# Kernel tuning notes

Measured on AMD Instinct MI355X. Metric: run time of the kernel, lower is better.

Reference implementation:

```python
import jax, jax.numpy as jnp
import numpy as np

SEM_DIM = 256
CODEBOOK_SIZE = 8192
FSQ_LEVELS = 21  # acoustic_codebook_size
EPS = 1e-5


def setup_inputs() -> dict:
    key = jax.random.key(0)
    k1, k2, k3 = jax.random.split(key, 3)
    x = jax.random.normal(k1, (8, 292, 4096), dtype=jnp.float32)
    embedding_sum = jax.random.normal(k2, (CODEBOOK_SIZE, SEM_DIM), dtype=jnp.float32)
    cluster_usage = jax.random.uniform(k3, (CODEBOOK_SIZE,), dtype=jnp.float32)
    return {"x": x, "embedding_sum": embedding_sum, "cluster_usage": cluster_usage}


def reference(x, embedding_sum, cluster_usage):
    B, D, T = x.shape
    # Codebook embedding = EMA sum / clamped usage  (SemanticCodebook.embedding)
    emb = embedding_sum / jnp.clip(cluster_usage, EPS, None)[:, None]  # [K, S]

    # ---- semantic encode: cdist(p=2) + argmin ----
    sem = x[:, :SEM_DIM, :]                                   # [B, S, T]
    flat = jnp.transpose(sem, (0, 2, 1)).reshape(B * T, SEM_DIM)  # [BT, S]
    x2 = jnp.sum(flat * flat, axis=-1, keepdims=True)         # [BT, 1]
    e2 = jnp.sum(emb * emb, axis=-1)                          # [K]
    d2 = x2 - 2.0 * (flat @ emb.T) + e2[None, :]              # [BT, K] squared dists
    sem_codes = jnp.argmin(d2, axis=-1).reshape(B, 1, T).astype(jnp.int64)

    # ---- acoustic encode: FSQ (tanh -> scale -> round) ----
    ac = jnp.tanh(x[:, SEM_DIM:, :])                          # [B, A, T]
    scaled = (ac + 1.0) * 0.5 * (FSQ_LEVELS - 1)
    ac_codes = jnp.round(scaled).astype(jnp.int64)            # [B, A, T]

    codes = jnp.concatenate([sem_codes, ac_codes], axis=1)    # [B, 1+A, T]

    # ---- decode (round trip) ----
    sem_emb = jnp.transpose(emb[sem_codes[:, 0, :]], (0, 2, 1))      # [B, S, T]
    ac_emb = ac_codes.astype(jnp.float32) * (2.0 / (FSQ_LEVELS - 1)) - 1.0  # [B, A, T]
    recon = jnp.concatenate([sem_emb, ac_emb], axis=1)        # [B, D, T]
    return codes, recon
```

## Files before the change

kernel.cpp:

```cpp
#include <hip/hip_runtime.h>
#include <hip/hip_bf16.h>

#define SEM_DIM   256
#define CODEBOOK  8192
#define B_        8
#define T_        4096
#define D_        292
#define NCH       37
#define EPSV      1e-5f
#define NSP       4
#define KAPPA     2.05e-3f
#define D0        0.01f
#define CAP       128
#define QMAX      1536

typedef unsigned short u16;
typedef float v4f __attribute__((ext_vector_type(4)));
typedef _Float16 v8h __attribute__((ext_vector_type(8)));

constexpr int ROWS = B_ * T_;
constexpr size_t OFF_XT   = 0;
constexpr size_t OFF_ET   = 4194304;
constexpr size_t OFF_E2G  = 5242880;
constexpr size_t OFF_X2   = 5259264;
constexpr size_t OFF_CNT  = 5292032;
constexpr size_t OFF_CAND = 5324800;
constexpr size_t RECON_OFF = 1212416;

__device__ __forceinline__ u16 h16bits(float v) {
    _Float16 h = (_Float16)v;
    return *(u16*)&h;
}

__global__ __launch_bounds__(256) void init_kernel(int* __restrict__ cnt,
                                                   float* __restrict__ x2)
{
    int r = blockIdx.x * 256 + threadIdx.x;
    cnt[r] = 0;
    x2[r] = 0.f;
}

__global__ __launch_bounds__(256) void prep_emb_kernel(
    const float* __restrict__ es, const float* __restrict__ cu,
    u16* __restrict__ Et, float* __restrict__ e2f, float* __restrict__ gf)
{
    int c = blockIdx.x;
    int d = threadIdx.x;
    float denom = fmaxf(cu[c], EPSV);
    float v = es[(size_t)c * SEM_DIM + d] / denom;
    float vc = fminf(fmaxf(v, -60000.f), 60000.f);

    __shared__ u16 hbuf[256];
    hbuf[d] = h16bits(vc);

    float s = v * v;
    #pragma unroll
    for (int m = 32; m >= 1; m >>= 1) s += __shfl_xor(s, m);
    __shared__ float red[4];
    int lane = d & 63, w = d >> 6;
    if (lane == 0) red[w] = s;
    __syncthreads();

    if (d < 32) {
        uint4 pk = *(const uint4*)&hbuf[d * 8];
        size_t byt = (size_t)(c >> 6) * 32768 + (size_t)d * 1024 + (size_t)(c & 63) * 16;
        *(uint4*)((char*)Et + byt) = pk;
    }
    if (d == 0) {
        float e2 = red[0] + red[1] + red[2] + red[3];
        e2f[c] = e2;
        gf[c]  = KAPPA * sqrtf(e2);
    }
}

__global__ __launch_bounds__(256) void prep_x_kernel(
    const float* __restrict__ x, u16* __restrict__ Xt, float* __restrict__ x2)
{
    __shared__ float tile[64][65];
    int bidx = blockIdx.x;
    int dc = bidx & 3;
    int tc = (bidx >> 2) & 63;
    int b  = bidx >> 8;
    int d0 = dc * 64, t0 = tc * 64;
    int tx = threadIdx.x & 63;
    int dq = threadIdx.x >> 6;

    float part = 0.f;
    #pragma unroll
    for (int i = 0; i < 16; i++) {
        int d = dq * 16 + i;
        float v = x[((size_t)b * D_ + d0 + d) * T_ + t0 + tx];
        tile[d][tx] = v;
        part = fmaf(v, v, part);
    }
    atomicAdd(&x2[b * T_ + t0 + tx], part);
    __syncthreads();

    #pragma unroll
    for (int j = 0; j < 2; j++) {
        int lin = threadIdx.x * 2 + j;
        int tr  = lin >> 3;
        int ch  = lin & 7;
        unsigned w[4];
        #pragma unroll
        for (int p = 0; p < 4; p++) {
            float v0 = tile[ch * 8 + p * 2 + 0][tr];
            float v1 = tile[ch * 8 + p * 2 + 1][tr];
            w[p] = (unsigned)h16bits(v0) | ((unsigned)h16bits(v1) << 16);
        }
        int row = b * T_ + t0 + tr;
        int R = row >> 4, l15 = row & 15;
        int k8 = d0 / 8 + ch;
        int ks = k8 >> 2, l4 = k8 & 3;
        size_t byt = (size_t)((R * 8 + ks) * 4 + l4) * 256 + (size_t)l15 * 16;
        *(uint4*)((char*)Xt + byt) = make_uint4(w[0], w[1], w[2], w[3]);
    }
}

#define GBM 256
#define NTT (CODEBOOK / NSP / 32)

__global__ __launch_bounds__(512, 4) void gemm_emit_kernel(
    const u16* __restrict__ Xt, const u16* __restrict__ Et,
    const float* __restrict__ e2f, const float* __restrict__ gf,
    const float* __restrict__ x2,
    int* __restrict__ cnt, u16* __restrict__ cand)
{
    __shared__ u16 Bs[2][8192];
    __shared__ float e2s[2048], gs[2048];
    __shared__ unsigned qbuf[QMAX];
    __shared__ int qn;
    int tid  = threadIdx.x;
    int lane = tid & 63, wid = tid >> 6;
    int l15 = lane & 15, l4 = lane >> 4;
    int mblk = blockIdx.x >> 2, split = blockIdx.x & 3;
    int m0 = mblk * GBM;
    int cbase = split * (CODEBOOK / NSP);
    if (tid == 0) qn = 0;

    {
        int c4 = tid * 4;
        *(float4*)&e2s[c4] = *(const float4*)&e2f[cbase + c4];
        *(float4*)&gs[c4]  = *(const float4*)&gf[cbase + c4];
    }

    v8h aX[2][8];
    #pragma unroll
    for (int mfm = 0; mfm < 2; mfm++) {
        int Rb = (m0 + wid * 32 + mfm * 16) >> 4;
        #pragma unroll
        for (int ks = 0; ks < 8; ks++) {
            size_t byt = (size_t)((Rb * 8 + ks) * 4 + l4) * 256 + (size_t)l15 * 16;
            aX[mfm][ks] = *(const v8h*)((const char*)Xt + byt);
        }
    }

    float sxv[2], rvL[2];
    #pragma unroll
    for (int mfm = 0; mfm < 2; mfm++) {
        sxv[mfm] = sqrtf(x2[m0 + wid * 32 + mfm * 16 + l15]);
        rvL[mfm] = 3.4e38f;
    }

    v4f acc[2][2];
    #pragma unroll
    for (int a = 0; a < 2; a++)
        #pragma unroll
        for (int b = 0; b < 2; b++)
            acc[a][b] = (v4f){0.f, 0.f, 0.f, 0.f};

    auto stage = [&](int nt, int buf) {
        const char* src = (const char*)Et
            + (size_t)(split * 32 + (nt >> 1)) * 32768 + (size_t)(nt & 1) * 512;
        #pragma unroll
        for (int j = 0; j < 2; j++) {
            int dofs = wid * 2048 + j * 1024 + lane * 16;
            int q = dofs >> 9;
            int o = (dofs >> 4) & 31;
            __builtin_amdgcn_global_load_lds(
                (const __attribute__((address_space(1))) unsigned*)(src + q * 1024 + o * 16),
                (__attribute__((address_space(3))) unsigned*)((char*)&Bs[buf][0] + dofs),
                16, 0, 0);
        }
    };

    stage(0, 0);

    for (int t = 0; t < NTT; ++t) {
        int buf = t & 1;
        __syncthreads();
        if (t + 1 < NTT) stage(t + 1, buf ^ 1);

        const char* bp = (const char*)&Bs[buf][0];
        #pragma unroll
        for (int ks = 0; ks < 8; ks++) {
            int cofs = (ks * 4 + l4) * 512 + l15 * 16;
            v8h bC0 = *(const v8h*)(bp + cofs);
            v8h bC1 = *(const v8h*)(bp + cofs + 256);
            #pragma unroll
            for (int mfm = 0; mfm < 2; mfm++) {
                acc[0][mfm] = __builtin_amdgcn_mfma_f32_16x16x32_f16(
                    bC0, aX[mfm][ks], acc[0][mfm], 0, 0, 0);
                acc[1][mfm] = __builtin_amdgcn_mfma_f32_16x16x32_f16(
                    bC1, aX[mfm][ks], acc[1][mfm], 0, 0, 0);
            }
        }

        int c0  = cbase + t * 32;
        int clb = t * 32 + l4 * 4;
        float4 e2q0 = *(const float4*)&e2s[clb];
        float4 e2q1 = *(const float4*)&e2s[clb + 16];
        float4 gq0  = *(const float4*)&gs[clb];
        float4 gq1  = *(const float4*)&gs[clb + 16];
        float e2a[2][4] = {{e2q0.x, e2q0.y, e2q0.z, e2q0.w},
                           {e2q1.x, e2q1.y, e2q1.z, e2q1.w}};
        float ga[2][4]  = {{gq0.x, gq0.y, gq0.z, gq0.w},
                           {gq1.x, gq1.y, gq1.z, gq1.w}};

        #pragma unroll
        for (int mfm = 0; mfm < 2; mfm++) {
            float sx = sxv[mfm];
            float om = 3.4e38f;
            float u[2][4];
            #pragma unroll
            for (int mfc = 0; mfc < 2; mfc++)
                #pragma unroll
                for (int rr = 0; rr < 4; rr++) {
                    float s = fmaf(-2.f, acc[mfc][mfm][rr], e2a[mfc][rr]);
                    om = fminf(om, fmaf(sx, ga[mfc][rr], s));
                    u[mfc][rr] = fmaf(-sx, ga[mfc][rr], s);
                }
            om = fminf(om, __shfl_xor(om, 16));
            om = fminf(om, __shfl_xor(om, 32));
            float rv = fminf(rvL[mfm], om);
            rvL[mfm] = rv;
            float th = rv + D0;
            int lrow = wid * 32 + mfm * 16 + l15;
            #pragma unroll
            for (int mfc = 0; mfc < 2; mfc++)
                #pragma unroll
                for (int rr = 0; rr < 4; rr++) {
                    if (u[mfc][rr] <= th) {
                        unsigned pk = ((unsigned)lrow << 13)
                                    | (unsigned)(c0 + mfc * 16 + l4 * 4 + rr);
                        int p = atomicAdd(&qn, 1);
                        if (p < QMAX) qbuf[p] = pk;
                        else {
                            int row = m0 + lrow;
                            int q = atomicAdd(&cnt[row], 1);
                            if (q < CAP) cand[(size_t)row * CAP + q] = (u16)(pk & 8191);
                        }
                    }
                }
        }
        #pragma unroll
        for (int a = 0; a < 2; a++)
            #pragma unroll
            for (int b = 0; b < 2; b++)
                acc[a][b] = (v4f){0.f, 0.f, 0.f, 0.f};
    }

    __syncthreads();
    int n = qn; if (n > QMAX) n = QMAX;
    for (int i = tid; i < n; i += 512) {
        unsigned pk = qbuf[i];
        int row = m0 + (pk >> 13);
        int q = atomicAdd(&cnt[row], 1);
        if (q < CAP) cand[(size_t)row * CAP + q] = (u16)(pk & 8191);
    }
}

__global__ __launch_bounds__(1024) void finalize_kernel(
    const int* __restrict__ cnt, const u16* __restrict__ cand,
    const float* __restrict__ x, const float* __restrict__ es,
    const float* __restrict__ cu, const float* __restrict__ e2f,
    float* __restrict__ out)
{
    int r = (blockIdx.x * 1024 + threadIdx.x) >> 6;
    int lane = threadIdx.x & 63;
    int b = r >> 12, t = r & 4095;
    int n = cnt[r];

    float xv[4];
    #pragma unroll
    for (int j = 0; j < 4; j++)
        xv[j] = x[((size_t)b * D_ + lane + j * 64) * T_ + t];

    float best_s = 3.4e38f; int best_i = 0x7FFFFFFF;
    if (n <= CAP) {
        for (int p = 0; p < n; p++) {
            int c = (int)cand[(size_t)r * CAP + p];
            float partial = 0.f;
            #pragma unroll
            for (int j = 0; j < 4; j++)
                partial = fmaf(xv[j], es[(size_t)c * SEM_DIM + lane + j * 64], partial);
            #pragma unroll
            for (int m = 32; m >= 1; m >>= 1) partial += __shfl_xor(partial, m);
            float sc = fmaf(-2.0f / fmaxf(cu[c], EPSV), partial, e2f[c]);
            if (sc < best_s || (sc == best_s && c < best_i)) { best_s = sc; best_i = c; }
        }
    } else {
        for (int c = 0; c < CODEBOOK; c++) {
            float partial = 0.f;
            #pragma unroll
            for (int j = 0; j < 4; j++)
                partial = fmaf(xv[j], es[(size_t)c * SEM_DIM + lane + j * 64], partial);
            #pragma unroll
            for (int m = 32; m >= 1; m <<= 1) partial += __shfl_xor(partial, m);
            float sc = fmaf(-2.0f / fmaxf(cu[c], EPSV), partial, e2f[c]);
            if (sc < best_s) { best_s = sc; best_i = c; }
        }
    }
    if (lane == 0) out[(size_t)b * NCH * T_ + t] = (float)best_i;
}

__global__ __launch_bounds__(256) void fsq_kernel(
    const float* __restrict__ x, float* __restrict__ out)
{
    int e = blockIdx.x * 256 + threadIdx.x;
    int t = e & 4095;
    int rest = e >> 12;
    int j = rest % 36;
    int b = rest / 36;
    float v = x[(size_t)b * D_ * T_ + (size_t)(SEM_DIM + j) * T_ + t];
    float a = tanhf(v);
    float code = rintf((a + 1.0f) * 10.0f);
    out[(size_t)b * NCH * T_ + (size_t)(1 + j) * T_ + t] = code;
    out[RECON_OFF + (size_t)b * D_ * T_ + (size_t)(SEM_DIM + j) * T_ + t]
        = code * 0.1f - 1.0f;
}

__global__ __launch_bounds__(256) void gather_kernel(
    const float* __restrict__ es, const float* __restrict__ cu,
    const float* __restrict__ codes, float* __restrict__ out)
{
    int bid = blockIdx.x;
    int b  = bid >> 6;
    int tc = bid & 63;
    int t  = tc * 64 + (threadIdx.x & 63);
    int w  = threadIdx.x >> 6;

    int c = (int)codes[(size_t)b * NCH * T_ + t];
    float denom = fmaxf(cu[c], EPSV);
    const float* erow = es + (size_t)c * SEM_DIM;
    float* orow = out + RECON_OFF + (size_t)b * D_ * T_ + t;

    #pragma unroll
    for (int i = 0; i < 16; i++) {
        int d = w * 64 + i * 4;
        float4 ev = *(const float4*)(erow + d);
        orow[(size_t)(d + 0) * T_] = ev.x / denom;
        orow[(size_t)(d + 1) * T_] = ev.y / denom;
        orow[(size_t)(d + 2) * T_] = ev.z / denom;
        orow[(size_t)(d + 3) * T_] = ev.w / denom;
    }
}

extern "C" void kernel_launch(void* const* d_in, const int* in_sizes, int n_in,
                              void* d_out, int out_size, void* d_ws, size_t ws_size,
                              hipStream_t stream)
{
    const float* x  = (const float*)d_in[0];
    const float* es = (const float*)d_in[1];
    const float* cu = (const float*)d_in[2];
    float* out = (float*)d_out;

    u16*   Xt   = (u16*)(out + OFF_XT);
    u16*   Et   = (u16*)(out + OFF_ET);
    float* e2f  = out + OFF_E2G;
    float* gf   = out + OFF_E2G + 8192;
    float* x2   = out + OFF_X2;
    int*   cnt  = (int*)(out + OFF_CNT);
    u16*   cand = (u16*)(out + OFF_CAND);

    init_kernel<<<ROWS / 256, 256, 0, stream>>>(cnt, x2);
    prep_emb_kernel<<<CODEBOOK, 256, 0, stream>>>(es, cu, Et, e2f, gf);
    prep_x_kernel<<<B_ * 64 * 4, 256, 0, stream>>>(x, Xt, x2);

    gemm_emit_kernel<<<(ROWS / GBM) * NSP, 512, 0, stream>>>(
        Xt, Et, e2f, gf, x2, cnt, cand);

    finalize_kernel<<<ROWS / 16, 1024, 0, stream>>>(cnt, cand, x, es, cu, e2f, out);

    fsq_kernel<<<(B_ * 36 * T_) / 256, 256, 0, stream>>>(x, out);

    gather_kernel<<<B_ * (T_ / 64), 256, 0, stream>>>(es, cu, out, out);
}
```

Baseline: 290.2 us.

## Triple-buffer codebook tiles with vmcnt waits and trim gemm LDS footprint

Moves the GEMM codebook staging from a double buffer with a full __syncthreads to a three-deep buffer. It waits on partial vmcnt and uses a bare s_barrier, so global-to-LDS loads for two tiles ahead overlap the MFMA work, and it raises wave priority around the MFMA loop. To pay for the extra LDS it stores the g-scale table as fp16 (slightly inflated to stay conservative) and halves the candidate queue. It also adds a per-row early-out before the emit loop, and folds the init kernel into prep_emb to drop one launch. The smaller queue may spill more candidates to global atomics, and the fp16 g values loosen the pruning bound a little.

New measurement: 382.8 us. 1.32x slower.

```diff
diff --git a/kernel.cpp b/kernel.cpp
--- a/kernel.cpp
+++ b/kernel.cpp
@@ -12,11 +12,12 @@
 #define KAPPA     2.05e-3f
 #define D0        0.01f
 #define CAP       128
-#define QMAX      1536
+#define QMAX      768
 
 typedef unsigned short u16;
 typedef float v4f __attribute__((ext_vector_type(4)));
 typedef _Float16 v8h __attribute__((ext_vector_type(8)));
+typedef _Float16 v4h __attribute__((ext_vector_type(4)));
 
 constexpr int ROWS = B_ * T_;
 constexpr size_t OFF_XT   = 0;
@@ -32,20 +33,16 @@
     return *(u16*)&h;
 }
 
-__global__ __launch_bounds__(256) void init_kernel(int* __restrict__ cnt,
-                                                   float* __restrict__ x2)
-{
-    int r = blockIdx.x * 256 + threadIdx.x;
-    cnt[r] = 0;
-    x2[r] = 0.f;
-}
-
 __global__ __launch_bounds__(256) void prep_emb_kernel(
     const float* __restrict__ es, const float* __restrict__ cu,
-    u16* __restrict__ Et, float* __restrict__ e2f, float* __restrict__ gf)
+    u16* __restrict__ Et, float* __restrict__ e2f, float* __restrict__ gf,
+    int* __restrict__ cnt, float* __restrict__ x2)
 {
     int c = blockIdx.x;
     int d = threadIdx.x;
+    if (c < 128)                  cnt[c * 256 + d] = 0;
+    else if (c < 256)             x2[(c - 128) * 256 + d] = 0.f;
+
     float denom = fmaxf(cu[c], EPSV);
     float v = es[(size_t)c * SEM_DIM + d] / denom;
     float vc = fminf(fmaxf(v, -60000.f), 60000.f);
@@ -126,8 +123,9 @@
     const float* __restrict__ x2,
     int* __restrict__ cnt, u16* __restrict__ cand)
 {
-    __shared__ u16 Bs[2][8192];
-    __shared__ float e2s[2048], gs[2048];
+    __shared__ u16 Bs[3][8192];
+    __shared__ float e2s[2048];
+    __shared__ _Float16 gs16[2048];
     __shared__ unsigned qbuf[QMAX];
     __shared__ int qn;
     int tid  = threadIdx.x;
@@ -140,8 +138,12 @@
 
     {
         int c4 = tid * 4;
-        *(float4*)&e2s[c4] = *(const float4*)&e2f[cbase + c4];
-        *(float4*)&gs[c4]  = *(const float4*)&gf[cbase + c4];
+        float4 e4 = *(const float4*)&e2f[cbase + c4];
+        float4 g4 = *(const float4*)&gf[cbase + c4];
+        *(float4*)&e2s[c4] = e4;
+        v4h gh = { (_Float16)(g4.x * 1.0005f), (_Float16)(g4.y * 1.0005f),
+                   (_Float16)(g4.z * 1.0005f), (_Float16)(g4.w * 1.0005f) };
+        *(v4h*)&gs16[c4] = gh;
     }
 
     v8h aX[2][8];
@@ -185,13 +187,17 @@
     };
 
     stage(0, 0);
+    stage(1, 1);
 
     for (int t = 0; t < NTT; ++t) {
-        int buf = t & 1;
-        __syncthreads();
-        if (t + 1 < NTT) stage(t + 1, buf ^ 1);
-
-        const char* bp = (const char*)&Bs[buf][0];
+        if (t < NTT - 1) asm volatile("s_waitcnt vmcnt(2)" ::: "memory");
+        else             asm volatile("s_waitcnt vmcnt(0)" ::: "memory");
+        __builtin_amdgcn_s_barrier();
+        asm volatile("" ::: "memory");
+        if (t + 2 < NTT) stage(t + 2, (t + 2) % 3);
+
+        const char* bp = (const char*)&Bs[t % 3][0];
+        __builtin_amdgcn_s_setprio(1);
         #pragma unroll
         for (int ks = 0; ks < 8; ks++) {
             int cofs = (ks * 4 + l4) * 512 + l15 * 16;
@@ -205,22 +211,23 @@
                     bC1, aX[mfm][ks], acc[1][mfm], 0, 0, 0);
             }
         }
+        __builtin_amdgcn_s_setprio(0);
 
         int c0  = cbase + t * 32;
         int clb = t * 32 + l4 * 4;
         float4 e2q0 = *(const float4*)&e2s[clb];
         float4 e2q1 = *(const float4*)&e2s[clb + 16];
-        float4 gq0  = *(const float4*)&gs[clb];
-        float4 gq1  = *(const float4*)&gs[clb + 16];
+        v4h gh0 = *(const v4h*)&gs16[clb];
+        v4h gh1 = *(const v4h*)&gs16[clb + 16];
         float e2a[2][4] = {{e2q0.x, e2q0.y, e2q0.z, e2q0.w},
                            {e2q1.x, e2q1.y, e2q1.z, e2q1.w}};
-        float ga[2][4]  = {{gq0.x, gq0.y, gq0.z, gq0.w},
-                           {gq1.x, gq1.y, gq1.z, gq1.w}};
+        float ga[2][4]  = {{(float)gh0[0], (float)gh0[1], (float)gh0[2], (float)gh0[3]},
+                           {(float)gh1[0], (float)gh1[1], (float)gh1[2], (float)gh1[3]}};
 
         #pragma unroll
         for (int mfm = 0; mfm < 2; mfm++) {
             float sx = sxv[mfm];
-            float om = 3.4e38f;
+            float om = 3.4e38f, umin = 3.4e38f;
             float u[2][4];
             #pragma unroll
             for (int mfc = 0; mfc < 2; mfc++)
@@ -228,30 +235,34 @@
                 for (int rr = 0; rr < 4; rr++) {
                     float s = fmaf(-2.f, acc[mfc][mfm][rr], e2a[mfc][rr]);
                     om = fminf(om, fmaf(sx, ga[mfc][rr], s));
-                    u[mfc][rr] = fmaf(-sx, ga[mfc][rr], s);
+                    float uu = fmaf(-sx, ga[mfc][rr], s);
+                    u[mfc][rr] = uu;
+                    umin = fminf(umin, uu);
                 }
             om = fminf(om, __shfl_xor(om, 16));
             om = fminf(om, __shfl_xor(om, 32));
             float rv = fminf(rvL[mfm], om);
             rvL[mfm] = rv;
             float th = rv + D0;
-            int lrow = wid * 32 + mfm * 16 + l15;
-            #pragma unroll
-            for (int mfc = 0; mfc < 2; mfc++)
+            if (umin <= th) {
+                int lrow = wid * 32 + mfm * 16 + l15;
                 #pragma unroll
-                for (int rr = 0; rr < 4; rr++) {
-                    if (u[mfc][rr] <= th) {
-                        unsigned pk = ((unsigned)lrow << 13)
-                                    | (unsigned)(c0 + mfc * 16 + l4 * 4 + rr);
-                        int p = atomicAdd(&qn, 1);
-                        if (p < QMAX) qbuf[p] = pk;
-                        else {
-                            int row = m0 + lrow;
-                            int q = atomicAdd(&cnt[row], 1);
-                            if (q < CAP) cand[(size_t)row * CAP + q] = (u16)(pk & 8191);
+                for (int mfc = 0; mfc < 2; mfc++)
+                    #pragma unroll
+                    for (int rr = 0; rr < 4; rr++) {
+                        if (u[mfc][rr] <= th) {
+                            unsigned pk = ((unsigned)lrow << 13)
+                                        | (unsigned)(c0 + mfc * 16 + l4 * 4 + rr);
+                            int p = atomicAdd(&qn, 1);
+                            if (p < QMAX) qbuf[p] = pk;
+                            else {
+                                int row = m0 + lrow;
+                                int q = atomicAdd(&cnt[row], 1);
+                                if (q < CAP) cand[(size_t)row * CAP + q] = (u16)(pk & 8191);
+                            }
                         }
                     }
-                }
+            }
         }
         #pragma unroll
         for (int a = 0; a < 2; a++)
@@ -373,8 +384,7 @@
     int*   cnt  = (int*)(out + OFF_CNT);
     u16*   cand = (u16*)(out + OFF_CAND);
 
-    init_kernel<<<ROWS / 256, 256, 0, stream>>>(cnt, x2);
-    prep_emb_kernel<<<CODEBOOK, 256, 0, stream>>>(es, cu, Et, e2f, gf);
+    prep_emb_kernel<<<CODEBOOK, 256, 0, stream>>>(es, cu, Et, e2f, gf, cnt, x2);
     prep_x_kernel<<<B_ * 64 * 4, 256, 0, stream>>>(x, Xt, x2);
 
     gemm_emit_kernel<<<(ROWS / GBM) * NSP, 512, 0, stream>>>(
```
